# Performance work log

Measured on AMD Instinct MI355X. Metric: run time of the kernel, lower is better.

## Reference

```python
import jax, jax.numpy as jnp
from jax import lax
import numpy as np

B, T, I, H = 512, 512, 128, 256


def setup_inputs() -> dict:
    key = jax.random.key(0)
    ks = jax.random.split(key, 7)
    s = 1.0 / np.sqrt(H)  # pytorch-style init scale
    return {
        "x": jax.random.normal(ks[0], (B, T, I), dtype=jnp.float32),
        "h0": jax.random.normal(ks[1], (1, B, H), dtype=jnp.float32),
        "c0": jax.random.normal(ks[2], (1, B, H), dtype=jnp.float32),
        "w_ih": jax.random.normal(ks[3], (4 * H, I), dtype=jnp.float32) * s,
        "w_hh": jax.random.normal(ks[4], (4 * H, H), dtype=jnp.float32) * s,
        "b_ih": jax.random.normal(ks[5], (4 * H,), dtype=jnp.float32) * s,
        "b_hh": jax.random.normal(ks[6], (4 * H,), dtype=jnp.float32) * s,
    }


def reference(x, h0, c0, w_ih, w_hh, b_ih, b_hh):
    """Single-layer LSTM; returns final cell state c_n of shape [1, B, H].
    Gate row order in w_*/b_* is PyTorch's (i, f, g, o) blocks of H."""
    h = h0[0]  # [B, H]
    c = c0[0]  # [B, H]
    # Precompute input contribution for all timesteps: [T, B, 4H]
    xg = jnp.einsum('bti,gi->tbg', x, w_ih) + (b_ih + b_hh)

    def step(carry, xg_t):
        h, c = carry
        g = xg_t + h @ w_hh.T  # [B, 4H]
        gi, gf, gg, go = jnp.split(g, 4, axis=-1)
        c_new = jax.nn.sigmoid(gf) * c + jax.nn.sigmoid(gi) * jnp.tanh(gg)
        h_new = jax.nn.sigmoid(go) * jnp.tanh(c_new)
        return (h_new, c_new), None

    (h_T, c_T), _ = lax.scan(step, (h, c), xg)
    return c_T[None]  # [1, B, H]
```

## Files before the change

### kernel.cpp

```cpp
#include <hip/hip_runtime.h>
#include <hip/hip_bf16.h>
#include <hip/hip_fp16.h>


typedef __attribute__((ext_vector_type(4))) float f32x4;
typedef __attribute__((ext_vector_type(8))) _Float16 f16x8;
typedef __attribute__((ext_vector_type(4))) unsigned int u32x4;
typedef __attribute__((ext_vector_type(4))) int i32x4;

static __device__ __forceinline__ float h2f(unsigned short u) {
  return (float)__builtin_bit_cast(_Float16, u);
}
static __device__ __forceinline__ unsigned short f2h(float f) {
  return __builtin_bit_cast(unsigned short, (_Float16)f);
}
static __device__ __forceinline__ float fast_sigmoid(float x) {
  return __builtin_amdgcn_rcpf(1.0f + __builtin_amdgcn_exp2f(-1.44269504f * x));
}
static __device__ __forceinline__ float fast_tanh(float x) {
  return 1.0f - 2.0f * __builtin_amdgcn_rcpf(1.0f + __builtin_amdgcn_exp2f(2.88539008f * x));
}

__global__ __launch_bounds__(256) void prep1(
    const float* __restrict__ whh, const float* __restrict__ h0,
    const float* __restrict__ wih, const float* __restrict__ bih,
    const float* __restrict__ bhh,
    float* __restrict__ scl, unsigned short* __restrict__ wih_h,
    float* __restrict__ bcv) {
  const int b = blockIdx.x, tid = threadIdx.x;
  if (b < 192) {
    __shared__ float s[256];
    const float* src = (b < 128) ? whh : h0;
    int base = (b < 128) ? b * 2048 : (b - 128) * 2048;
    float m = 0.f;
#pragma unroll
    for (int i = 0; i < 8; ++i) m = fmaxf(m, fabsf(src[base + i * 256 + tid]));
    s[tid] = m; __syncthreads();
    for (int w = 128; w > 0; w >>= 1) {
      if (tid < w) s[tid] = fmaxf(s[tid], s[tid + w]);
      __syncthreads();
    }
    if (tid == 0) scl[8 + b] = s[0];
  } else {
    int i = ((b - 192) * 256 + tid) * 4;
    int q = i >> 7, k = i & 127;
    int p = (q & 3) * 256 + (q >> 2);
    f32x4 v = *(const f32x4*)(wih + p * 128 + k);
    ushort4 pk;
    pk.x = f2h(v[0]); pk.y = f2h(v[1]); pk.z = f2h(v[2]); pk.w = f2h(v[3]);
    *(ushort4*)(wih_h + i) = pk;
    if (b == 192) {
      for (int q2 = tid; q2 < 1024; q2 += 256) {
        int p2 = (q2 & 3) * 256 + (q2 >> 2);
        bcv[q2] = bih[p2] + bhh[p2];
      }
    }
  }
}

__global__ __launch_bounds__(256) void prep2(
    const float* __restrict__ whh, const float* __restrict__ h0,
    const float* __restrict__ c0, float* __restrict__ scl,
    signed char* __restrict__ wq, signed char* __restrict__ hst,
    float* __restrict__ cst) {
  __shared__ float s[256];
  const int b = blockIdx.x, tid = threadIdx.x;
  float v = (tid < 128) ? scl[8 + tid] : 0.f;
  s[tid] = v; __syncthreads();
  for (int w = 128; w > 0; w >>= 1) {
    if (tid < w) s[tid] = fmaxf(s[tid], s[tid + w]);
    __syncthreads();
  }
  float sw = s[0]; __syncthreads();
  v = (tid < 64) ? scl[136 + tid] : 0.f;
  s[tid] = v; __syncthreads();
  for (int w = 128; w > 0; w >>= 1) {
    if (tid < w) s[tid] = fmaxf(s[tid], s[tid + w]);
    __syncthreads();
  }
  float sh = s[0];
  if (b == 0 && tid == 0) { scl[0] = sw; scl[1] = sh; }

  const float invw = 127.0f / sw;
  int base = b * 1024;
#pragma unroll
  for (int i = 0; i < 4; ++i) {
    int idx = base + i * 256 + tid;
    int nr = idx >> 8, k = idx & 255;
    int g = nr >> 8, r = nr & 255;
    int wvv = r >> 5, ntc = (r >> 4) & 1, cc = r & 15;
    int src = g * 256 + wvv * 32 + 2 * cc + ntc;
    int q = (int)rintf(whh[src * 256 + k] * invw);
    wq[idx] = (signed char)max(-127, min(127, q));
  }
  const float invh = 127.0f / sh;
  int sb = b * 512;
#pragma unroll
  for (int i = 0; i < 2; ++i) {
    int idx = sb + i * 256 + tid;
    int q = (int)rintf(h0[idx] * invh);
    hst[idx] = (signed char)max(-127, min(127, q));
    cst[idx] = c0[idx];
  }
}

__global__ __launch_bounds__(256) void xgemm(
    const float* __restrict__ x, const unsigned short* __restrict__ wih,
    const float* __restrict__ bconv,
    unsigned short* __restrict__ xg, int t0, int tclog) {
  __shared__ unsigned short Ash[128 * 128];
  __shared__ unsigned short Bsh[128 * 128];

  const int tid  = threadIdx.x;
  const int lane = tid & 63;
  const int wv   = tid >> 6;
  const int c16  = lane & 15;
  const int gq   = lane >> 4;
  const long m0  = (long)blockIdx.x * 128;
  const int tcm  = (1 << tclog) - 1;

#pragma unroll
  for (int i = 0; i < 16; ++i) {
    int fidx = (i * 256 + tid) * 4;
    int row = fidx >> 7, k = fidx & 127;
    long cr = m0 + row;
    long b  = cr >> tclog;
    long tl = cr & tcm;
    f32x4 v = *(const f32x4*)(x + ((size_t)b * 512 + t0 + tl) * 128 + k);
    ushort4 pk;
    pk.x = f2h(v[0]); pk.y = f2h(v[1]); pk.z = f2h(v[2]); pk.w = f2h(v[3]);
    int byte = (row * 256 + k * 2) ^ ((row & 7) << 4);
    *(ushort4*)((char*)Ash + byte) = pk;
  }

  const int mh = (wv >> 1) * 64;
  const int nh = (wv & 1) * 64;

  for (int nc = 0; nc < 8; ++nc) {
    __syncthreads();
    {
      const char* wb = (const char*)(wih + nc * 128 * 128);
#pragma unroll
      for (int i = 0; i < 8; ++i) {
        int idx16 = i * 256 + tid;
        int row = idx16 >> 4, ch = idx16 & 15;
        int srcoff = row * 256 + ((ch * 16) ^ ((row & 7) << 4));
        u32x4 v = *(const u32x4*)(wb + srcoff);
        *(u32x4*)((char*)Bsh + idx16 * 16) = v;
      }
    }
    __syncthreads();

    float bias_v[4];
#pragma unroll
    for (int nt = 0; nt < 4; ++nt)
      bias_v[nt] = bconv[nc * 128 + nh + nt * 16 + c16];

    f16x8 af[4][4], bfr[4][4];
#pragma unroll
    for (int sm = 0; sm < 4; ++sm)
#pragma unroll
      for (int kt = 0; kt < 4; ++kt) {
        int m = mh + sm * 16 + c16;
        int byte = (m * 256 + (kt * 32 + gq * 8) * 2) ^ ((m & 7) << 4);
        af[sm][kt] = __builtin_bit_cast(f16x8, *(const u32x4*)((const char*)Ash + byte));
      }
#pragma unroll
    for (int nt = 0; nt < 4; ++nt)
#pragma unroll
      for (int kt = 0; kt < 4; ++kt) {
        int n = nh + nt * 16 + c16;
        int byte = (n * 256 + (kt * 32 + gq * 8) * 2) ^ ((n & 7) << 4);
        bfr[nt][kt] = __builtin_bit_cast(f16x8, *(const u32x4*)((const char*)Bsh + byte));
      }

    f32x4 acc[4][4];
#pragma unroll
    for (int sm = 0; sm < 4; ++sm)
#pragma unroll
      for (int nt = 0; nt < 4; ++nt) { f32x4 z = {0.f, 0.f, 0.f, 0.f}; acc[sm][nt] = z; }
#pragma unroll
    for (int sm = 0; sm < 4; ++sm)
#pragma unroll
      for (int nt = 0; nt < 4; ++nt)
#pragma unroll
        for (int kt = 0; kt < 4; ++kt)
          acc[sm][nt] = __builtin_amdgcn_mfma_f32_16x16x32_f16(af[sm][kt], bfr[nt][kt], acc[sm][nt], 0, 0, 0);

#pragma unroll
    for (int sm = 0; sm < 4; ++sm)
#pragma unroll
      for (int nt = 0; nt < 4; ++nt) {
        long row = m0 + mh + sm * 16 + gq * 4;
        int gcol = nc * 128 + nh + nt * 16 + c16;
#pragma unroll
        for (int r = 0; r < 4; ++r)
          xg[(size_t)(row + r) * 1024 + gcol] = f2h(acc[sm][nt][r] + bias_v[nt]);
      }
  }
}

__global__ __launch_bounds__(512)
void fused_chunk(
    const unsigned short* __restrict__ xgc, const signed char* __restrict__ wq,
    const float* __restrict__ scales, signed char* __restrict__ hst,
    float* __restrict__ cst, float* __restrict__ out, int Tc, int first, int last,
    const float* __restrict__ x, const unsigned short* __restrict__ wih,
    const float* __restrict__ bconv, unsigned short* __restrict__ xgn,
    int t0n, int tclog, int do_x) {
  __shared__ char smem[65536];

  const int tid  = threadIdx.x;
  const int lane = tid & 63;
  const int wv   = tid >> 6;
  const int c16  = lane & 15;
  const int gq   = lane >> 4;

  if (blockIdx.x < 128) {
    signed char (*hb)[1152] = (signed char (*)[1152])smem;
    const int b0 = blockIdx.x * 4;

    const int colA = wv * 32 + 2 * c16;
    float2 cv = *(const float2*)&cst[(b0 + gq) * 256 + colA];

    const float sw   = scales[0] * (1.0f / 127.0f);
    const float facR = sw * (1.0f / 127.0f);
    const float fac0 = first ? sw * (scales[1] * (1.0f / 127.0f)) : facR;

    i32x4 wf[8][4];
#pragma unroll
    for (int nt = 0; nt < 8; ++nt)
#pragma unroll
      for (int kt = 0; kt < 4; ++kt) {
        int n = (nt >> 1) * 256 + wv * 32 + (nt & 1) * 16 + c16;
        wf[nt][kt] = *(const i32x4*)(wq + n * 256 + kt * 64 + gq * 16);
      }
#pragma unroll
    for (int nt = 0; nt < 8; ++nt)
#pragma unroll
      for (int kt = 0; kt < 4; ++kt)
        asm volatile("" : "+v"(wf[nt][kt]));
    asm volatile("" ::: "memory");

    for (int i = tid; i < 1024; i += 512) {
      int row = i >> 8, cc = i & 255;
      hb[0][row * 288 + cc] = hst[(b0 + row) * 256 + cc];
    }

    const char* pxp = (const char*)xgc +
        (((size_t)(b0 + gq) * Tc) * 1024 + (size_t)colA * 4) * 2;
    u32x4 px = *(const u32x4*)pxp;
    pxp += 2048;

    const bool mrow = (c16 & 3) == 0;
    const int  hrow = c16 >> 2;
    i32x4 af[4];
#pragma unroll
    for (int kt = 0; kt < 4; ++kt) { i32x4 z = {0, 0, 0, 0}; af[kt] = z; }
    const i32x4 zacc = {0, 0, 0, 0};
    unsigned short hpack = 0;

    __syncthreads();

    for (int tt = 0; tt < Tc; ++tt) {
      const int cur = tt & 1;

      if (mrow) {
        const signed char* hp = &hb[cur][hrow * 288 + gq * 16];
        af[0] = *(const i32x4*)(hp);
        af[1] = *(const i32x4*)(hp + 64);
        af[2] = *(const i32x4*)(hp + 128);
        af[3] = *(const i32x4*)(hp + 192);
      }

      u32x4 pn = *(const u32x4*)pxp;
      pxp += 2048;

      i32x4 acc[8];
#pragma unroll
      for (int ne = 0; ne < 4; ++ne)
        acc[2 * ne] = __builtin_amdgcn_mfma_i32_16x16x64_i8(af[0], wf[2 * ne][0], zacc, 0, 0, 0);
#pragma unroll
      for (int kt = 1; kt < 4; ++kt)
#pragma unroll
        for (int ne = 0; ne < 4; ++ne)
          acc[2 * ne] = __builtin_amdgcn_mfma_i32_16x16x64_i8(af[kt], wf[2 * ne][kt], acc[2 * ne], 0, 0, 0);
#pragma unroll
      for (int ne = 0; ne < 4; ++ne)
        acc[2 * ne + 1] = __builtin_amdgcn_mfma_i32_16x16x64_i8(af[0], wf[2 * ne + 1][0], zacc, 0, 0, 0);
#pragma unroll
      for (int kt = 1; kt < 4; ++kt)
#pragma unroll
        for (int ne = 0; ne < 4; ++ne)
          acc[2 * ne + 1] = __builtin_amdgcn_mfma_i32_16x16x64_i8(af[kt], wf[2 * ne + 1][kt], acc[2 * ne + 1], 0, 0, 0);

      const float fac = (tt == 0) ? fac0 : facR;

      int q0, q1;
      {
        float gi = __builtin_fmaf((float)acc[0][0], fac, h2f((unsigned short)(px[0] & 0xffff)));
        float gf = __builtin_fmaf((float)acc[2][0], fac, h2f((unsigned short)(px[0] >> 16)));
        float gg = __builtin_fmaf((float)acc[4][0], fac, h2f((unsigned short)(px[1] & 0xffff)));
        float go = __builtin_fmaf((float)acc[6][0], fac, h2f((unsigned short)(px[1] >> 16)));
        cv.x = fast_sigmoid(gf) * cv.x + fast_sigmoid(gi) * fast_tanh(gg);
        float hn = fast_sigmoid(go) * fast_tanh(cv.x);
        q0 = (int)rintf(hn * 127.0f);
      }
      {
        float gi = __builtin_fmaf((float)acc[1][0], fac, h2f((unsigned short)(px[2] & 0xffff)));
        float gf = __builtin_fmaf((float)acc[3][0], fac, h2f((unsigned short)(px[2] >> 16)));
        float gg = __builtin_fmaf((float)acc[5][0], fac, h2f((unsigned short)(px[3] & 0xffff)));
        float go = __builtin_fmaf((float)acc[7][0], fac, h2f((unsigned short)(px[3] >> 16)));
        cv.y = fast_sigmoid(gf) * cv.y + fast_sigmoid(gi) * fast_tanh(gg);
        float hn = fast_sigmoid(go) * fast_tanh(cv.y);
        q1 = (int)rintf(hn * 127.0f);
      }
      hpack = (unsigned short)((q0 & 0xff) | ((q1 & 0xff) << 8));
      *(unsigned short*)&hb[cur ^ 1][gq * 288 + colA] = hpack;

      px = pn;
      __syncthreads();
    }

    *(float2*)&cst[(b0 + gq) * 256 + colA] = cv;
    *(unsigned short*)&hst[(b0 + gq) * 256 + colA] = hpack;
    if (last) {
      *(float2*)&out[(b0 + gq) * 256 + colA] = cv;
    }
  } else if (do_x) {
    unsigned short* Ash = (unsigned short*)smem;
    unsigned short* Bsh = (unsigned short*)(smem + 32768);
    const int tcm    = (1 << tclog) - 1;
    const int ntiles = Tc << 2;
    const int wm = wv >> 2, wn = wv & 3;
    const int mh = wm * 64, nh = wn * 32;

    for (int rt = (int)blockIdx.x - 128; rt < ntiles; rt += 128) {
      const long m0 = (long)rt * 128;
      __syncthreads();

#pragma unroll
      for (int i = 0; i < 8; ++i) {
        int fidx = (i * 512 + tid) * 4;
        int row = fidx >> 7, k = fidx & 127;
        long cr = m0 + row;
        long b  = cr >> tclog;
        long tl = cr & tcm;
        f32x4 v = *(const f32x4*)(x + ((size_t)b * 512 + t0n + tl) * 128 + k);
        ushort4 pk;
        pk.x = f2h(v[0]); pk.y = f2h(v[1]); pk.z = f2h(v[2]); pk.w = f2h(v[3]);
        int byte = (row * 256 + k * 2) ^ ((row & 7) << 4);
        *(ushort4*)((char*)Ash + byte) = pk;
      }

      for (int nc = 0; nc < 8; ++nc) {
        __syncthreads();
        {
          const char* wb = (const char*)(wih + nc * 128 * 128);
#pragma unroll
          for (int i = 0; i < 4; ++i) {
            int idx16 = i * 512 + tid;
            int row = idx16 >> 4, ch = idx16 & 15;
            int srcoff = row * 256 + ((ch * 16) ^ ((row & 7) << 4));
            u32x4 v = *(const u32x4*)(wb + srcoff);
            *(u32x4*)((char*)Bsh + idx16 * 16) = v;
          }
        }
        __syncthreads();

        float bias_v[2];
#pragma unroll
        for (int nt = 0; nt < 2; ++nt)
          bias_v[nt] = bconv[nc * 128 + nh + nt * 16 + c16];

        f16x8 af[4][4], bfr[2][4];
#pragma unroll
        for (int sm = 0; sm < 4; ++sm)
#pragma unroll
          for (int kt = 0; kt < 4; ++kt) {
            int m = mh + sm * 16 + c16;
            int byte = (m * 256 + (kt * 32 + gq * 8) * 2) ^ ((m & 7) << 4);
            af[sm][kt] = __builtin_bit_cast(f16x8, *(const u32x4*)((const char*)Ash + byte));
          }
#pragma unroll
        for (int nt = 0; nt < 2; ++nt)
#pragma unroll
          for (int kt = 0; kt < 4; ++kt) {
            int n = nh + nt * 16 + c16;
            int byte = (n * 256 + (kt * 32 + gq * 8) * 2) ^ ((n & 7) << 4);
            bfr[nt][kt] = __builtin_bit_cast(f16x8, *(const u32x4*)((const char*)Bsh + byte));
          }

        f32x4 acc[4][2];
#pragma unroll
        for (int sm = 0; sm < 4; ++sm)
#pragma unroll
          for (int nt = 0; nt < 2; ++nt) { f32x4 z = {0.f, 0.f, 0.f, 0.f}; acc[sm][nt] = z; }
#pragma unroll
        for (int sm = 0; sm < 4; ++sm)
#pragma unroll
          for (int nt = 0; nt < 2; ++nt)
#pragma unroll
            for (int kt = 0; kt < 4; ++kt)
              acc[sm][nt] = __builtin_amdgcn_mfma_f32_16x16x32_f16(af[sm][kt], bfr[nt][kt], acc[sm][nt], 0, 0, 0);

#pragma unroll
        for (int sm = 0; sm < 4; ++sm)
#pragma unroll
          for (int nt = 0; nt < 2; ++nt) {
            long row = m0 + mh + sm * 16 + gq * 4;
            int gcol = nc * 128 + nh + nt * 16 + c16;
#pragma unroll
            for (int r = 0; r < 4; ++r)
              xgn[(size_t)(row + r) * 1024 + gcol] = f2h(acc[sm][nt][r] + bias_v[nt]);
          }
      }
    }
  }
}

extern "C" void kernel_launch(void* const* d_in, const int* in_sizes, int n_in,
                              void* d_out, int out_size, void* d_ws, size_t ws_size,
                              hipStream_t stream) {
  const float* x   = (const float*)d_in[0];
  const float* h0  = (const float*)d_in[1];
  const float* c0  = (const float*)d_in[2];
  const float* wih = (const float*)d_in[3];
  const float* whh = (const float*)d_in[4];
  const float* bih = (const float*)d_in[5];
  const float* bhh = (const float*)d_in[6];
  float* out = (float*)d_out;

  const size_t fixed = 262144u  + 262144u  + 131072u
                     + 524288u  + 4096u  + 1024u ;
  int tc = 128;
  while (tc > 4 && 2u * (size_t)512 * tc * 2048 + fixed > ws_size) tc >>= 1;
  int tclog = 31 - __builtin_clz((unsigned)tc);
  size_t bufsz = (size_t)512 * tc * 2048;

  char* ws = (char*)d_ws;
  unsigned short* xgb0  = (unsigned short*)ws;
  unsigned short* xgb1  = (unsigned short*)(ws + bufsz);
  size_t off = 2u * bufsz;
  unsigned short* wih_h = (unsigned short*)(ws + off);  off += 262144u;
  signed char*    wqb   = (signed char*)(ws + off);     off += 262144u;
  signed char*    hst   = (signed char*)(ws + off);     off += 131072u;
  float*          cst   = (float*)(ws + off);           off += 524288u;
  float*          bcv   = (float*)(ws + off);           off += 4096u;
  float*          scl   = (float*)(ws + off);

  prep1<<<320, 256, 0, stream>>>(whh, h0, wih, bih, bhh, scl, wih_h, bcv);
  prep2<<<256, 256, 0, stream>>>(whh, h0, c0, scl, wqb, hst, cst);

  xgemm<<<4 * tc, 256, 0, stream>>>(x, wih_h, bcv, xgb0, 0, tclog);

  int NC = 512 / tc;
  for (int c = 0; c < NC; ++c) {
    unsigned short* cur = (c & 1) ? xgb1 : xgb0;
    unsigned short* nxt = (c & 1) ? xgb0 : xgb1;
    int do_x = (c + 1 < NC) ? 1 : 0;
    fused_chunk<<<256, 512, 0, stream>>>(
        cur, wqb, scl, hst, cst, out, tc, (c == 0) ? 1 : 0, (c == NC - 1) ? 1 : 0,
        x, wih_h, bcv, nxt, (c + 1) * tc, tclog, do_x);
  }
}
```

Before: 526.2 us.

## Double workgroup size to 1024 threads, one hidden column per lane in recurrence

The fused recurrent kernel now launches 1024-thread blocks, so each wave handles 16 hidden columns with 4 gate MFMA chains instead of 32 columns with 8. The weight quantization layout is simplified to plain row order to match the new column mapping, and the xgemm branch halves its per-wave M tile to spread the same work over 16 waves. The aim is to shorten the serial per-timestep MFMA and activation chain by spreading it across more waves. In exchange, block-wide barriers now synchronize twice as many waves every timestep.

```diff
diff --git a/kernel.cpp b/kernel.cpp
--- a/kernel.cpp
+++ b/kernel.cpp
@@ -86,11 +86,7 @@
 #pragma unroll
   for (int i = 0; i < 4; ++i) {
     int idx = base + i * 256 + tid;
-    int nr = idx >> 8, k = idx & 255;
-    int g = nr >> 8, r = nr & 255;
-    int wvv = r >> 5, ntc = (r >> 4) & 1, cc = r & 15;
-    int src = g * 256 + wvv * 32 + 2 * cc + ntc;
-    int q = (int)rintf(whh[src * 256 + k] * invw);
+    int q = (int)rintf(whh[idx] * invw);
     wq[idx] = (signed char)max(-127, min(127, q));
   }
   const float invh = 127.0f / sh;
@@ -200,7 +196,7 @@
   }
 }
 
-__global__ __launch_bounds__(512)
+__global__ __launch_bounds__(1024)
 void fused_chunk(
     const unsigned short* __restrict__ xgc, const signed char* __restrict__ wq,
     const float* __restrict__ scales, signed char* __restrict__ hst,
@@ -219,37 +215,33 @@
   if (blockIdx.x < 128) {
     signed char (*hb)[1152] = (signed char (*)[1152])smem;
     const int b0 = blockIdx.x * 4;
-
-    const int colA = wv * 32 + 2 * c16;
-    float2 cv = *(const float2*)&cst[(b0 + gq) * 256 + colA];
+    const int col = wv * 16 + c16;
+    float cv = cst[(b0 + gq) * 256 + col];
 
     const float sw   = scales[0] * (1.0f / 127.0f);
     const float facR = sw * (1.0f / 127.0f);
     const float fac0 = first ? sw * (scales[1] * (1.0f / 127.0f)) : facR;
 
-    i32x4 wf[8][4];
-#pragma unroll
-    for (int nt = 0; nt < 8; ++nt)
-#pragma unroll
-      for (int kt = 0; kt < 4; ++kt) {
-        int n = (nt >> 1) * 256 + wv * 32 + (nt & 1) * 16 + c16;
-        wf[nt][kt] = *(const i32x4*)(wq + n * 256 + kt * 64 + gq * 16);
-      }
-#pragma unroll
-    for (int nt = 0; nt < 8; ++nt)
+    i32x4 wf[4][4];
+#pragma unroll
+    for (int g = 0; g < 4; ++g)
 #pragma unroll
       for (int kt = 0; kt < 4; ++kt)
-        asm volatile("" : "+v"(wf[nt][kt]));
-    asm volatile("" ::: "memory");
-
-    for (int i = tid; i < 1024; i += 512) {
-      int row = i >> 8, cc = i & 255;
+        wf[g][kt] = *(const i32x4*)(wq + (g * 256 + col) * 256 + kt * 64 + gq * 16);
+#pragma unroll
+    for (int g = 0; g < 4; ++g)
+#pragma unroll
+      for (int kt = 0; kt < 4; ++kt)
+        asm volatile("" : "+v"(wf[g][kt]));
+
+    {
+      int row = tid >> 8, cc = tid & 255;
       hb[0][row * 288 + cc] = hst[(b0 + row) * 256 + cc];
     }
 
     const char* pxp = (const char*)xgc +
-        (((size_t)(b0 + gq) * Tc) * 1024 + (size_t)colA * 4) * 2;
-    u32x4 px = *(const u32x4*)pxp;
+        (((size_t)(b0 + gq) * Tc) * 1024 + (size_t)col * 4) * 2;
+    uint2 px = *(const uint2*)pxp;
     pxp += 2048;
 
     const bool mrow = (c16 & 3) == 0;
@@ -258,7 +250,7 @@
 #pragma unroll
     for (int kt = 0; kt < 4; ++kt) { i32x4 z = {0, 0, 0, 0}; af[kt] = z; }
     const i32x4 zacc = {0, 0, 0, 0};
-    unsigned short hpack = 0;
+    int qlast = 0;
 
     __syncthreads();
 
@@ -273,75 +265,59 @@
         af[3] = *(const i32x4*)(hp + 192);
       }
 
-      u32x4 pn = *(const u32x4*)pxp;
+      uint2 pn = *(const uint2*)pxp;
       pxp += 2048;
 
-      i32x4 acc[8];
-#pragma unroll
-      for (int ne = 0; ne < 4; ++ne)
-        acc[2 * ne] = __builtin_amdgcn_mfma_i32_16x16x64_i8(af[0], wf[2 * ne][0], zacc, 0, 0, 0);
-#pragma unroll
-      for (int kt = 1; kt < 4; ++kt)
-#pragma unroll
-        for (int ne = 0; ne < 4; ++ne)
-          acc[2 * ne] = __builtin_amdgcn_mfma_i32_16x16x64_i8(af[kt], wf[2 * ne][kt], acc[2 * ne], 0, 0, 0);
-#pragma unroll
-      for (int ne = 0; ne < 4; ++ne)
-        acc[2 * ne + 1] = __builtin_amdgcn_mfma_i32_16x16x64_i8(af[0], wf[2 * ne + 1][0], zacc, 0, 0, 0);
-#pragma unroll
-      for (int kt = 1; kt < 4; ++kt)
-#pragma unroll
-        for (int ne = 0; ne < 4; ++ne)
-          acc[2 * ne + 1] = __builtin_amdgcn_mfma_i32_16x16x64_i8(af[kt], wf[2 * ne + 1][kt], acc[2 * ne + 1], 0, 0, 0);
+      i32x4 acc[4];
+      {
+        const int go_[4] = {2, 0, 1, 3};
+#pragma unroll
+        for (int gi_ = 0; gi_ < 4; ++gi_) {
+          const int g = go_[gi_];
+          acc[g] = __builtin_amdgcn_mfma_i32_16x16x64_i8(af[0], wf[g][0], zacc, 0, 0, 0);
+#pragma unroll
+          for (int kt = 1; kt < 4; ++kt)
+            acc[g] = __builtin_amdgcn_mfma_i32_16x16x64_i8(af[kt], wf[g][kt], acc[g], 0, 0, 0);
+        }
+      }
 
       const float fac = (tt == 0) ? fac0 : facR;
 
-      int q0, q1;
-      {
-        float gi = __builtin_fmaf((float)acc[0][0], fac, h2f((unsigned short)(px[0] & 0xffff)));
-        float gf = __builtin_fmaf((float)acc[2][0], fac, h2f((unsigned short)(px[0] >> 16)));
-        float gg = __builtin_fmaf((float)acc[4][0], fac, h2f((unsigned short)(px[1] & 0xffff)));
-        float go = __builtin_fmaf((float)acc[6][0], fac, h2f((unsigned short)(px[1] >> 16)));
-        cv.x = fast_sigmoid(gf) * cv.x + fast_sigmoid(gi) * fast_tanh(gg);
-        float hn = fast_sigmoid(go) * fast_tanh(cv.x);
-        q0 = (int)rintf(hn * 127.0f);
-      }
-      {
-        float gi = __builtin_fmaf((float)acc[1][0], fac, h2f((unsigned short)(px[2] & 0xffff)));
-        float gf = __builtin_fmaf((float)acc[3][0], fac, h2f((unsigned short)(px[2] >> 16)));
-        float gg = __builtin_fmaf((float)acc[5][0], fac, h2f((unsigned short)(px[3] & 0xffff)));
-        float go = __builtin_fmaf((float)acc[7][0], fac, h2f((unsigned short)(px[3] >> 16)));
-        cv.y = fast_sigmoid(gf) * cv.y + fast_sigmoid(gi) * fast_tanh(gg);
-        float hn = fast_sigmoid(go) * fast_tanh(cv.y);
-        q1 = (int)rintf(hn * 127.0f);
-      }
-      hpack = (unsigned short)((q0 & 0xff) | ((q1 & 0xff) << 8));
-      *(unsigned short*)&hb[cur ^ 1][gq * 288 + colA] = hpack;
+      float xi  = h2f((unsigned short)(px.x & 0xffff));
+      float xf  = h2f((unsigned short)(px.x >> 16));
+      float xgv = h2f((unsigned short)(px.y & 0xffff));
+      float xo  = h2f((unsigned short)(px.y >> 16));
+      float gi = __builtin_fmaf((float)acc[0][0], fac, xi);
+      float gf = __builtin_fmaf((float)acc[1][0], fac, xf);
+      float gg = __builtin_fmaf((float)acc[2][0], fac, xgv);
+      float go = __builtin_fmaf((float)acc[3][0], fac, xo);
+      cv = fast_sigmoid(gf) * cv + fast_sigmoid(gi) * fast_tanh(gg);
+      float hn = fast_sigmoid(go) * fast_tanh(cv);
+      qlast = (int)rintf(hn * 127.0f);
+      hb[cur ^ 1][gq * 288 + col] = (signed char)qlast;
 
       px = pn;
       __syncthreads();
     }
 
-    *(float2*)&cst[(b0 + gq) * 256 + colA] = cv;
-    *(unsigned short*)&hst[(b0 + gq) * 256 + colA] = hpack;
-    if (last) {
-      *(float2*)&out[(b0 + gq) * 256 + colA] = cv;
-    }
+    cst[(b0 + gq) * 256 + col] = cv;
+    hst[(b0 + gq) * 256 + col] = (signed char)qlast;
+    if (last) out[(b0 + gq) * 256 + col] = cv;
   } else if (do_x) {
     unsigned short* Ash = (unsigned short*)smem;
     unsigned short* Bsh = (unsigned short*)(smem + 32768);
     const int tcm    = (1 << tclog) - 1;
     const int ntiles = Tc << 2;
     const int wm = wv >> 2, wn = wv & 3;
-    const int mh = wm * 64, nh = wn * 32;
+    const int mh = wm * 32, nh = wn * 32;
 
     for (int rt = (int)blockIdx.x - 128; rt < ntiles; rt += 128) {
       const long m0 = (long)rt * 128;
       __syncthreads();
 
 #pragma unroll
-      for (int i = 0; i < 8; ++i) {
-        int fidx = (i * 512 + tid) * 4;
+      for (int i = 0; i < 4; ++i) {
+        int fidx = (i * 1024 + tid) * 4;
         int row = fidx >> 7, k = fidx & 127;
         long cr = m0 + row;
         long b  = cr >> tclog;
@@ -358,8 +334,8 @@
         {
           const char* wb = (const char*)(wih + nc * 128 * 128);
 #pragma unroll
-          for (int i = 0; i < 4; ++i) {
-            int idx16 = i * 512 + tid;
+          for (int i = 0; i < 2; ++i) {
+            int idx16 = i * 1024 + tid;
             int row = idx16 >> 4, ch = idx16 & 15;
             int srcoff = row * 256 + ((ch * 16) ^ ((row & 7) << 4));
             u32x4 v = *(const u32x4*)(wb + srcoff);
@@ -373,9 +349,9 @@
         for (int nt = 0; nt < 2; ++nt)
           bias_v[nt] = bconv[nc * 128 + nh + nt * 16 + c16];
 
-        f16x8 af[4][4], bfr[2][4];
-#pragma unroll
-        for (int sm = 0; sm < 4; ++sm)
+        f16x8 af[2][4], bfr[2][4];
+#pragma unroll
+        for (int sm = 0; sm < 2; ++sm)
 #pragma unroll
           for (int kt = 0; kt < 4; ++kt) {
             int m = mh + sm * 16 + c16;
@@ -391,13 +367,13 @@
             bfr[nt][kt] = __builtin_bit_cast(f16x8, *(const u32x4*)((const char*)Bsh + byte));
           }
 
-        f32x4 acc[4][2];
-#pragma unroll
-        for (int sm = 0; sm < 4; ++sm)
+        f32x4 acc[2][2];
+#pragma unroll
+        for (int sm = 0; sm < 2; ++sm)
 #pragma unroll
           for (int nt = 0; nt < 2; ++nt) { f32x4 z = {0.f, 0.f, 0.f, 0.f}; acc[sm][nt] = z; }
 #pragma unroll
-        for (int sm = 0; sm < 4; ++sm)
+        for (int sm = 0; sm < 2; ++sm)
 #pragma unroll
           for (int nt = 0; nt < 2; ++nt)
 #pragma unroll
@@ -405,7 +381,7 @@
               acc[sm][nt] = __builtin_amdgcn_mfma_f32_16x16x32_f16(af[sm][kt], bfr[nt][kt], acc[sm][nt], 0, 0, 0);
 
 #pragma unroll
-        for (int sm = 0; sm < 4; ++sm)
+        for (int sm = 0; sm < 2; ++sm)
 #pragma unroll
           for (int nt = 0; nt < 2; ++nt) {
             long row = m0 + mh + sm * 16 + gq * 4;
@@ -459,7 +435,7 @@
     unsigned short* cur = (c & 1) ? xgb1 : xgb0;
     unsigned short* nxt = (c & 1) ? xgb0 : xgb1;
     int do_x = (c + 1 < NC) ? 1 : 0;
-    fused_chunk<<<256, 512, 0, stream>>>(
+    fused_chunk<<<256, 1024, 0, stream>>>(
         cur, wqb, scl, hst, cst, out, tc, (c == 0) ? 1 : 0, (c == NC - 1) ? 1 : 0,
         x, wih_h, bcv, nxt, (c + 1) * tc, tclog, do_x);
   }
```

New measurement: 522.6 us. About the same (-0.7%).
